# Kernel tuning notes

Hardware: AMD Instinct MI355X
Metric: run time of the kernel (lower is better)

The kernel has to match this reference:

```python
import jax, jax.numpy as jnp
import numpy as np

N_EMBED = 1024
N_HEAD = 16
D = N_EMBED // N_HEAD
B, T = 2, 2048
EPS = 1e-5


def _layer_norm(x, w, b):
    mu = jnp.mean(x, axis=-1, keepdims=True)
    var = jnp.mean(jnp.square(x - mu), axis=-1, keepdims=True)
    return (x - mu) * jax.lax.rsqrt(var + EPS) * w + b


def setup_inputs() -> dict:
    key = jax.random.key(0)
    ks = jax.random.split(key, 13)
    E = N_EMBED
    s_attn = 1.0 / np.sqrt(E)
    s_fc = 1.0 / np.sqrt(E)
    s_proj = 1.0 / np.sqrt(4 * E)
    return {
        "x": jax.random.normal(ks[0], (B, T, E), jnp.float32),
        "ln1_w": jnp.ones((E,), jnp.float32),
        "ln1_b": jnp.ones((E,), jnp.float32),
        "w_qkv": jax.random.normal(ks[1], (E, 3 * E), jnp.float32) * s_attn,
        "b_qkv": jax.random.normal(ks[2], (3 * E,), jnp.float32) * 0.02,
        "w_o": jax.random.normal(ks[3], (E, E), jnp.float32) * s_attn,
        "b_o": jax.random.normal(ks[4], (E,), jnp.float32) * 0.02,
        "ln2_w": jnp.ones((E,), jnp.float32),
        "ln2_b": jnp.ones((E,), jnp.float32),
        "w_fc": jax.random.normal(ks[5], (E, 4 * E), jnp.float32) * s_fc,
        "b_fc": jax.random.normal(ks[6], (4 * E,), jnp.float32) * 0.02,
        "w_proj": jax.random.normal(ks[7], (4 * E, E), jnp.float32) * s_proj,
        "b_proj": jax.random.normal(ks[8], (E,), jnp.float32) * 0.02,
    }


def reference(x, ln1_w, ln1_b, w_qkv, b_qkv, w_o, b_o, ln2_w, ln2_b, w_fc, b_fc, w_proj, b_proj):
    Bb, Tt, E = x.shape
    # --- attention branch ---
    h = _layer_norm(x, ln1_w, ln1_b)
    qkv = h @ w_qkv + b_qkv                         # [B,T,3E]
    q, k, v = jnp.split(qkv, 3, axis=-1)
    q = q.reshape(Bb, Tt, N_HEAD, D).transpose(0, 2, 1, 3)  # [B,H,T,D]
    k = k.reshape(Bb, Tt, N_HEAD, D).transpose(0, 2, 1, 3)
    v = v.reshape(Bb, Tt, N_HEAD, D).transpose(0, 2, 1, 3)
    scale = 1.0 / np.sqrt(D)
    a = scale * jnp.einsum("bhqd,bhkd->bhqk", q, k)  # [B,H,T,T]
    causal = jnp.tril(jnp.ones((Tt, Tt), bool))
    a = jnp.where(causal, a, -jnp.inf)
    a = jax.nn.softmax(a, axis=-1)
    y = jnp.einsum("bhqk,bhkd->bhqd", a, v)          # [B,H,T,D]
    y = y.transpose(0, 2, 1, 3).reshape(Bb, Tt, E)
    y = y @ w_o + b_o
    x = x + y
    # --- MLP branch ---
    h = _layer_norm(x, ln2_w, ln2_b)
    h = jax.nn.gelu(h @ w_fc + b_fc, approximate=False)
    h = h @ w_proj + b_proj
    return x + h
```

## Files before the change

kernel.cpp:

```cpp
#include <hip/hip_runtime.h>
#include <cstdint>
#include <cstddef>

#define E 1024
#define TT 2048
#define NB 2
#define NH 16
#define HD 64

using u16 = unsigned short;
using bf16x8 = __attribute__((ext_vector_type(8))) __bf16;
using floatx4 = __attribute__((ext_vector_type(4))) float;
using s16x4 = __attribute__((ext_vector_type(4))) short;

__device__ __forceinline__ float b2f(u16 u) {
  unsigned int x = ((unsigned int)u) << 16;
  float f;
  __builtin_memcpy(&f, &x, 4);
  return f;
}
__device__ __forceinline__ u16 f2b(float f) {
  unsigned int x;
  __builtin_memcpy(&x, &f, 4);
  x += 0x7fffu + ((x >> 16) & 1u);
  return (u16)(x >> 16);
}
__device__ __forceinline__ u16 f2b_fast(float f) {
  unsigned int x;
  float g = f * 1.001953125f;
  __builtin_memcpy(&x, &g, 4);
  return (u16)(x >> 16);
}

__device__ __forceinline__ void async16(const u16* g, u16* l) {
  __builtin_amdgcn_global_load_lds(
      (const __attribute__((address_space(1))) unsigned int*)g,
      (__attribute__((address_space(3))) unsigned int*)l, 16, 0, 0);
}

__device__ __forceinline__ floatx4 mfma32(bf16x8 a, bf16x8 b, floatx4 c) {
  return __builtin_amdgcn_mfma_f32_16x16x32_bf16(a, b, c, 0, 0, 0);
}

__device__ __forceinline__ floatx4 mfma16(s16x4 a, s16x4 b, floatx4 c) {
#if defined(__HIP_DEVICE_COMPILE__)
  return __builtin_amdgcn_mfma_f32_16x16x16bf16_1k(a, b, c, 0, 0, 0);
#else
  return c;
#endif
}

__global__ __launch_bounds__(256) void wconv_all(
    const float* __restrict__ w0, const float* __restrict__ w1,
    const float* __restrict__ w2, const float* __restrict__ w3,
    u16* __restrict__ o0, u16* __restrict__ o1, u16* __restrict__ o2,
    u16* __restrict__ o3) {
  __shared__ float tile[32][33];
  const int t = blockIdx.x;
  const float* w;
  u16* o;
  int K, N, nx, ti;
  if (t < 3072) { w = w0; o = o0; K = 1024; N = 3072; nx = 96; ti = t; }
  else if (t < 4096) { w = w1; o = o1; K = 1024; N = 1024; nx = 32; ti = t - 3072; }
  else if (t < 8192) { w = w2; o = o2; K = 1024; N = 4096; nx = 128; ti = t - 4096; }
  else { w = w3; o = o3; K = 4096; N = 1024; nx = 32; ti = t - 8192; }
  const int n0 = (ti % nx) * 32, k0 = (ti / nx) * 32;
  const int tx = threadIdx.x, ty = threadIdx.y;
#pragma unroll
  for (int i = 0; i < 32; i += 8)
    tile[ty + i][tx] = w[(size_t)(k0 + ty + i) * N + (n0 + tx)];
  __syncthreads();
#pragma unroll
  for (int i = 0; i < 32; i += 8)
    o[(size_t)(n0 + ty + i) * K + (k0 + tx)] = f2b(tile[tx][ty + i]);
}

__global__ __launch_bounds__(256) void ln_kernel(const float* __restrict__ x,
                                                 const float* __restrict__ w,
                                                 const float* __restrict__ bvec,
                                                 u16* __restrict__ outb) {
  const int row = blockIdx.x;
  const int t = threadIdx.x;
  const float4 v = ((const float4*)(x + (size_t)row * E))[t];
  float s1 = v.x + v.y + v.z + v.w;
  float s2 = v.x * v.x + v.y * v.y + v.z * v.z + v.w * v.w;
#pragma unroll
  for (int off = 32; off > 0; off >>= 1) {
    s1 += __shfl_down(s1, off);
    s2 += __shfl_down(s2, off);
  }
  __shared__ float r1[4], r2[4];
  if ((t & 63) == 0) { r1[t >> 6] = s1; r2[t >> 6] = s2; }
  __syncthreads();
  s1 = r1[0] + r1[1] + r1[2] + r1[3];
  s2 = r2[0] + r2[1] + r2[2] + r2[3];
  const float mean = s1 * (1.f / E);
  const float var = s2 * (1.f / E) - mean * mean;
  const float rstd = rsqrtf(var + 1e-5f);
  const float4 wv = ((const float4*)w)[t];
  const float4 bv = ((const float4*)bvec)[t];
  const u16 o0 = f2b((v.x - mean) * rstd * wv.x + bv.x);
  const u16 o1 = f2b((v.y - mean) * rstd * wv.y + bv.y);
  const u16 o2 = f2b((v.z - mean) * rstd * wv.z + bv.z);
  const u16 o3 = f2b((v.w - mean) * rstd * wv.w + bv.w);
  uint2 pk;
  pk.x = (unsigned)o0 | ((unsigned)o1 << 16);
  pk.y = (unsigned)o2 | ((unsigned)o3 << 16);
  ((uint2*)(outb + (size_t)row * E))[t] = pk;
}

template <int MODE, int ROWS>
__global__ __launch_bounds__(512) void gemm_bt(const u16* __restrict__ A,
                                               const u16* __restrict__ BT,
                                               const float* __restrict__ bias,
                                               const float* __restrict__ res,
                                               void* __restrict__ outp,
                                               int M, int N, int K) {
  constexpr int NJ = (ROWS == 256) ? 4 : 2;
  __shared__ __align__(16) u16 As[2][ROWS * 32];
  __shared__ __align__(16) u16 Bs[2][128 * 32];
  const int tid = threadIdx.x;
  const int wave = tid >> 6, lane = tid & 63;

  const int gx = gridDim.x, gy = gridDim.y;
  const int L = blockIdx.y * gx + blockIdx.x;
  const int xc = L & 7, wi = L >> 3;
  const int cpg = gx >> 2;
  const int rpg = gy >> 1;
  const int bxs = (xc >> 1) * cpg + (wi % cpg);
  const int bys = (xc & 1) * rpg + (wi / cpg);

  const int row0 = bys * ROWS, col0 = bxs * 128;
  const int wm = (ROWS == 256) ? (wave & 3) * 64 : (wave & 1) * 64;
  const int wn = (ROWS == 256) ? (wave >> 2) * 64 : (wave >> 1) * 32;
  const int r = lane & 15, qd = lane >> 4;

  floatx4 acc[4][NJ];
#pragma unroll
  for (int i = 0; i < 4; i++)
#pragma unroll
    for (int j = 0; j < NJ; j++) acc[i][j] = (floatx4){0.f, 0.f, 0.f, 0.f};

  const int cA0 = tid, cA1 = tid + 512, cB = tid;
  const u16* ApA = A + (size_t)(row0 + (cA0 >> 2)) * K + (cA0 & 3) * 8;
  const u16* ApB = A + (size_t)(row0 + (cA1 >> 2)) * K + (cA1 & 3) * 8;
  const u16* Bp = BT + (size_t)(col0 + (cB >> 2)) * K + (cB & 3) * 8;

  auto stage = [&](int kt, u16* Asb, u16* Bsb) {
    async16(ApA + kt, Asb + cA0 * 8);
    if (ROWS == 256) async16(ApB + kt, Asb + cA1 * 8);
    async16(Bp + kt, Bsb + cB * 8);
  };
  auto compute = [&](const u16* Asb, const u16* Bsb) {
    bf16x8 af[4], bfr[NJ];
#pragma unroll
    for (int i = 0; i < 4; i++)
      af[i] = *(const bf16x8*)&Asb[(wm + i * 16 + r) * 32 + qd * 8];
#pragma unroll
    for (int j = 0; j < NJ; j++)
      bfr[j] = *(const bf16x8*)&Bsb[(wn + j * 16 + r) * 32 + qd * 8];
#pragma unroll
    for (int i = 0; i < 4; i++)
#pragma unroll
      for (int j = 0; j < NJ; j++)
        acc[i][j] = mfma32(af[i], bfr[j], acc[i][j]);
  };

  const int nIter = K >> 5;
  stage(0, As[0], Bs[0]);
  for (int t = 0; t < nIter; t++) {
    const int tb = t & 1;
    if (t + 1 < nIter) {
      stage((t + 1) * 32, As[tb ^ 1], Bs[tb ^ 1]);
      if (ROWS == 256)
        asm volatile("s_waitcnt vmcnt(3)" ::: "memory");
      else
        asm volatile("s_waitcnt vmcnt(2)" ::: "memory");
    } else {
      asm volatile("s_waitcnt vmcnt(0)" ::: "memory");
    }
    asm volatile("s_barrier" ::: "memory");
    compute(As[tb], Bs[tb]);
    asm volatile("s_barrier" ::: "memory");
  }

#pragma unroll
  for (int i = 0; i < 4; i++) {
#pragma unroll
    for (int j = 0; j < NJ; j++) {
      const int col = col0 + wn + j * 16 + r;
      const float bc = bias[col];
      if (MODE == 3) {
        u16* base = (u16*)outp;
        const int rowb = row0 + wm + i * 16 + qd * 4;
        if (col < 2048) {
          const size_t cb =
              (col < 1024) ? (size_t)col : ((size_t)4096 * 1024 + (col - 1024));
#pragma unroll
          for (int rr = 0; rr < 4; rr++)
            base[cb + (size_t)(rowb + rr) * 1024] = f2b(acc[i][j][rr] + bc);
        } else {
          ushort4 pk;
          pk.x = f2b(acc[i][j][0] + bc);
          pk.y = f2b(acc[i][j][1] + bc);
          pk.z = f2b(acc[i][j][2] + bc);
          pk.w = f2b(acc[i][j][3] + bc);
          *(ushort4*)(base + (size_t)8 * 1024 * 1024 +
                      (size_t)(col - 2048) * 4096 + rowb) = pk;
        }
      } else {
#pragma unroll
        for (int rr = 0; rr < 4; rr++) {
          const int row = row0 + wm + i * 16 + qd * 4 + rr;
          const float v = acc[i][j][rr] + bc;
          const size_t idx = (size_t)row * N + col;
          if (MODE == 0) {
            ((u16*)outp)[idx] = f2b(v);
          } else if (MODE == 1) {
            ((float*)outp)[idx] = v + res[idx];
          } else {
            const float z = 1.5957691216f * v * (1.f + 0.044715f * v * v);
            const float g = v / (1.f + __expf(-z));
            ((u16*)outp)[idx] = f2b(g);
          }
        }
      }
    }
  }
}

__global__ __launch_bounds__(512) void gemm_ks(const u16* __restrict__ A,
                                               const u16* __restrict__ BT,
                                               const float* __restrict__ bias,
                                               const float* __restrict__ res,
                                               float* __restrict__ outp,
                                               int M, int N, int K) {
  __shared__ __align__(16) u16 As[4][2][128 * 32];
  __shared__ __align__(16) u16 Bs[4][2][128 * 32];
  const int tid = threadIdx.x;
  const int wave = tid >> 6, lane = tid & 63;

  const int gx = gridDim.x, gy = gridDim.y;
  const int L = blockIdx.y * gx + blockIdx.x;
  const int xc = L & 7, wi = L >> 3;
  const int cpg = gx >> 2, rpg = gy >> 1;
  const int bxs = (xc >> 1) * cpg + (wi % cpg);
  const int bys = (xc & 1) * rpg + (wi / cpg);

  const int row0 = bys * 128, col0 = bxs * 128;
  const int kg = wave >> 2;
  const int wm = (wave & 1) * 64, wn = ((wave >> 1) & 1) * 64;
  const int r = lane & 15, qd = lane >> 4;

  floatx4 acc[4][4];
#pragma unroll
  for (int i = 0; i < 4; i++)
#pragma unroll
    for (int j = 0; j < 4; j++) acc[i][j] = (floatx4){0.f, 0.f, 0.f, 0.f};

  const int arow = tid >> 2, aslot = (tid & 3) * 8;
  const u16* Ap = A + (size_t)(row0 + arow) * K + aslot;
  const u16* Bp = BT + (size_t)(col0 + arow) * K + aslot;

  auto stage = [&](int s, int d) {
    const int k0 = s * 64;
    async16(Ap + k0, &As[d][0][tid * 8]);
    async16(Ap + k0 + 32, &As[d][1][tid * 8]);
    async16(Bp + k0, &Bs[d][0][tid * 8]);
    async16(Bp + k0 + 32, &Bs[d][1][tid * 8]);
  };
  auto compute = [&](int d) {
    bf16x8 af[4], bfr[4];
#pragma unroll
    for (int i = 0; i < 4; i++)
      af[i] = *(const bf16x8*)&As[d][kg][(wm + i * 16 + r) * 32 + qd * 8];
#pragma unroll
    for (int j = 0; j < 4; j++)
      bfr[j] = *(const bf16x8*)&Bs[d][kg][(wn + j * 16 + r) * 32 + qd * 8];
#pragma unroll
    for (int i = 0; i < 4; i++)
#pragma unroll
      for (int j = 0; j < 4; j++)
        acc[i][j] = mfma32(af[i], bfr[j], acc[i][j]);
  };

  const int nT = K >> 6;
  stage(0, 0);
  stage(1, 1);
  stage(2, 2);
  for (int tt = 0; tt < nT; tt += 4) {
#pragma unroll
    for (int d = 0; d < 4; d++) {
      const int t = tt + d;
      const int rem = nT - 1 - t;
      if (rem >= 2)
        asm volatile("s_waitcnt vmcnt(8)" ::: "memory");
      else if (rem == 1)
        asm volatile("s_waitcnt vmcnt(4)" ::: "memory");
      else
        asm volatile("s_waitcnt vmcnt(0)" ::: "memory");
      asm volatile("s_barrier" ::: "memory");
      if (t + 3 < nT) stage(t + 3, (d + 3) & 3);
      compute(d);
    }
  }

  __syncthreads();
  float* S = (float*)&As[0][0][0];
  const int p = wave & 3;
  floatx4* W = (floatx4*)S + p * 1024 + lane;
  if (kg == 1) {
#pragma unroll
    for (int i = 0; i < 4; i++)
#pragma unroll
      for (int j = 0; j < 4; j++) W[(i * 4 + j) * 64] = acc[i][j];
  }
  __syncthreads();
  if (kg == 0) {
#pragma unroll
    for (int i = 0; i < 4; i++) {
#pragma unroll
      for (int j = 0; j < 4; j++) {
        const floatx4 w2 = W[(i * 4 + j) * 64];
        const int col = col0 + wn + j * 16 + r;
        const float bc = bias[col];
#pragma unroll
        for (int rr = 0; rr < 4; rr++) {
          const int row = row0 + wm + i * 16 + qd * 4 + rr;
          const size_t idx = (size_t)row * N + col;
          outp[idx] = acc[i][j][rr] + w2[rr] + bc + res[idx];
        }
      }
    }
  }
}

__global__ __launch_bounds__(512, 4) void attn_mfma(const u16* __restrict__ qb,
                                                    const u16* __restrict__ kb,
                                                    const u16* __restrict__ vtb,
                                                    u16* __restrict__ y) {
  const int bx = blockIdx.x;
  const int h = blockIdx.y, b = blockIdx.z;
  const int qt = b ? (15 - bx) : bx;
  const int tid = threadIdx.x;
  const int wave = tid >> 6, lane = tid & 63;
  const int quad = lane >> 4, r = lane & 15;
  const int wq = wave & 3;
  const int kvh = wave >> 2;

  __shared__ __align__(16) u16 lds[2 * 128 * 64 + 2 * 64 * 128];
  u16* KsB = lds;
  u16* VsB = lds + 2 * 128 * 64;

  const float C = 0.125f * 1.44269504f;
  const int qbase = qt * 128 + wq * 32;

  bf16x8 qf[2][2];
#pragma unroll
  for (int f = 0; f < 2; f++) {
    const u16* qp = qb + ((size_t)b * TT + qbase + f * 16 + r) * E + h * 64;
#pragma unroll
    for (int kh = 0; kh < 2; kh++) {
      union { bf16x8 v; u16 u[8]; } tmp;
#pragma unroll
      for (int j = 0; j < 8; j++) tmp.u[j] = f2b(b2f(qp[kh * 32 + quad * 8 + j]) * C);
      qf[f][kh] = tmp.v;
    }
  }

  floatx4 o[2][4];
#pragma unroll
  for (int f = 0; f < 2; f++)
#pragma unroll
    for (int i = 0; i < 4; i++) o[f][i] = (floatx4){0.f, 0.f, 0.f, 0.f};
  float lsum[2] = {0.f, 0.f};
  const bool mgt[4] = {(quad * 4 + 0) > r, (quad * 4 + 1) > r,
                       (quad * 4 + 2) > r, (quad * 4 + 3) > r};

  auto stageKV = [&](int it, int bi) {
    const int k0 = it * 128;
    u16* Kd = KsB + bi * (128 * 64);
    u16* Vd = VsB + bi * (64 * 128);
#pragma unroll
    for (int i = 0; i < 2; i++) {
      const int c = tid + i * 512;
      const int key = c >> 3, dc = (c & 7) ^ (key & 7);
      async16(kb + ((size_t)b * TT + k0 + key) * E + h * 64 + dc * 8, Kd + c * 8);
    }
#pragma unroll
    for (int i = 0; i < 2; i++) {
      const int c = tid + i * 512;
      const int d = c >> 4, kc = (c & 15) ^ (d & 15);
      async16(vtb + (size_t)(h * 64 + d) * (NB * TT) + b * TT + k0 + kc * 8,
              Vd + c * 8);
    }
  };

  const int nIter = qt + 1;
  stageKV(0, 0);
  for (int it = 0; it < nIter; it++) {
    if (it + 1 < nIter) {
      stageKV(it + 1, (it + 1) & 1);
      asm volatile("s_waitcnt vmcnt(4)" ::: "memory");
    } else {
      asm volatile("s_waitcnt vmcnt(0)" ::: "memory");
    }
    asm volatile("s_barrier" ::: "memory");
    const u16* Kb = KsB + (it & 1) * (128 * 64);
    const u16* Vb = VsB + (it & 1) * (64 * 128);
    const int k0 = it * 128;
    const int relA = (qbase - k0) >> 4;
    const int kTop = (relA + 1 < 7) ? (relA + 1) : 7;

#pragma unroll
    for (int kk = 0; kk < 4; kk++) {
      const int ks = kvh * 4 + kk;
      if (ks <= kTop) {
        const int key = ks * 16 + r, kx = key & 7;
        const bf16x8 kf0 = *(const bf16x8*)&Kb[key * 64 + (quad ^ kx) * 8];
        const bf16x8 kf1 = *(const bf16x8*)&Kb[key * 64 + ((4 + quad) ^ kx) * 8];
        floatx4 s0 = (floatx4){0.f, 0.f, 0.f, 0.f};
        s0 = mfma32(kf0, qf[0][0], s0);
        s0 = mfma32(kf1, qf[0][1], s0);
        floatx4 s1 = (floatx4){0.f, 0.f, 0.f, 0.f};
        s1 = mfma32(kf0, qf[1][0], s1);
        s1 = mfma32(kf1, qf[1][1], s1);

        s16x4 vf[4];
#pragma unroll
        for (int dsub = 0; dsub < 4; dsub++) {
          const int d = dsub * 16 + r;
          vf[dsub] = *(const s16x4*)&Vb[d * 128 + ((2 * ks + (quad >> 1)) ^ r) * 8 +
                                        (quad & 1) * 4];
        }

#pragma unroll
        for (int f = 0; f < 2; f++) {
          const floatx4 sv = (f == 0) ? s0 : s1;
          const int rel = relA + f;
          if (ks <= rel) {
            float p0 = exp2f(sv[0]);
            float p1 = exp2f(sv[1]);
            float p2 = exp2f(sv[2]);
            float p3 = exp2f(sv[3]);
            if (ks == rel) {
              if (mgt[0]) p0 = 0.f;
              if (mgt[1]) p1 = 0.f;
              if (mgt[2]) p2 = 0.f;
              if (mgt[3]) p3 = 0.f;
            }
            lsum[f] += p0 + p1 + p2 + p3;
            s16x4 pk;
            pk[0] = (short)f2b_fast(p0);
            pk[1] = (short)f2b_fast(p1);
            pk[2] = (short)f2b_fast(p2);
            pk[3] = (short)f2b_fast(p3);
#pragma unroll
            for (int dsub = 0; dsub < 4; dsub++)
              o[f][dsub] = mfma16(pk, vf[dsub], o[f][dsub]);
          }
        }
      }
    }
    asm volatile("s_barrier" ::: "memory");
  }

  floatx4* W = (floatx4*)(float*)lds + wq * 576 + lane;
  if (kvh == 1) {
#pragma unroll
    for (int f = 0; f < 2; f++)
#pragma unroll
      for (int dsub = 0; dsub < 4; dsub++) W[(f * 4 + dsub) * 64] = o[f][dsub];
    W[8 * 64] = (floatx4){lsum[0], lsum[1], 0.f, 0.f};
  }
  __syncthreads();
  if (kvh == 0) {
    const floatx4 ls2 = W[8 * 64];
#pragma unroll
    for (int f = 0; f < 2; f++) {
      float lv = lsum[f] + ((f == 0) ? ls2[0] : ls2[1]);
      lv += __shfl_xor(lv, 16);
      lv += __shfl_xor(lv, 32);
      float linv[4];
#pragma unroll
      for (int rr = 0; rr < 4; rr++) linv[rr] = 1.f / __shfl(lv, quad * 4 + rr);
#pragma unroll
      for (int dsub = 0; dsub < 4; dsub++) {
        const floatx4 o2 = W[(f * 4 + dsub) * 64];
#pragma unroll
        for (int rr = 0; rr < 4; rr++) {
          const size_t row = (size_t)b * TT + qbase + f * 16 + quad * 4 + rr;
          y[row * E + h * 64 + dsub * 16 + r] =
              f2b((o[f][dsub][rr] + o2[rr]) * linv[rr]);
        }
      }
    }
  }
}

extern "C" void kernel_launch(void* const* d_in, const int* in_sizes, int n_in,
                              void* d_out, int out_size, void* d_ws, size_t ws_size,
                              hipStream_t stream) {
  (void)in_sizes; (void)n_in; (void)out_size; (void)ws_size;
  const float* x      = (const float*)d_in[0];
  const float* ln1w   = (const float*)d_in[1];
  const float* ln1b   = (const float*)d_in[2];
  const float* w_qkv  = (const float*)d_in[3];
  const float* b_qkv  = (const float*)d_in[4];
  const float* w_o    = (const float*)d_in[5];
  const float* b_o    = (const float*)d_in[6];
  const float* ln2w   = (const float*)d_in[7];
  const float* ln2b   = (const float*)d_in[8];
  const float* w_fc   = (const float*)d_in[9];
  const float* b_fc   = (const float*)d_in[10];
  const float* w_proj = (const float*)d_in[11];
  const float* b_proj = (const float*)d_in[12];
  float* out = (float*)d_out;

  char* p = (char*)d_ws;
  u16* wT_qkv  = (u16*)p; p += (size_t)3072 * 1024 * 2;
  u16* wT_o    = (u16*)p; p += (size_t)1024 * 1024 * 2;
  u16* wT_fc   = (u16*)p; p += (size_t)4096 * 1024 * 2;
  u16* wT_proj = (u16*)p; p += (size_t)1024 * 4096 * 2;
  u16* hbuf    = (u16*)p; p += (size_t)4096 * 1024 * 2;
  u16* qkvb    = (u16*)p; p += (size_t)4096 * 3072 * 2;
  float* x2    = (float*)p; p += (size_t)4096 * 1024 * 4;
  u16* gbuf    = (u16*)p; p += (size_t)4096 * 4096 * 2;

  u16* qb  = qkvb;
  u16* kb  = qkvb + (size_t)4096 * 1024;
  u16* vtb = qkvb + (size_t)8 * 1024 * 1024;

  wconv_all<<<12288, dim3(32, 8), 0, stream>>>(w_qkv, w_o, w_fc, w_proj,
                                               wT_qkv, wT_o, wT_fc, wT_proj);

  ln_kernel<<<4096, 256, 0, stream>>>(x, ln1w, ln1b, hbuf);
  gemm_bt<3, 256><<<dim3(3072 / 128, 4096 / 256), 512, 0, stream>>>(
      hbuf, wT_qkv, b_qkv, nullptr, qkvb, 4096, 3072, 1024);
  attn_mfma<<<dim3(16, NH, NB), 512, 0, stream>>>(qb, kb, vtb, hbuf);
  gemm_ks<<<dim3(1024 / 128, 4096 / 128), 512, 0, stream>>>(
      hbuf, wT_o, b_o, x, x2, 4096, 1024, 1024);
  ln_kernel<<<4096, 256, 0, stream>>>(x2, ln2w, ln2b, hbuf);
  gemm_bt<2, 256><<<dim3(4096 / 128, 4096 / 256), 512, 0, stream>>>(
      hbuf, wT_fc, b_fc, nullptr, gbuf, 4096, 4096, 1024);
  gemm_ks<<<dim3(1024 / 128, 4096 / 128), 512, 0, stream>>>(
      gbuf, wT_proj, b_proj, x2, out, 4096, 1024, 4096);
}
```

Baseline: 319.1 us.

## Split-K the output-projection GEMMs across grid z with atomic accumulation

The gemm_ks kernel now splits K in half across blockIdx.z, doubling the block count for the N=1024 GEMMs (from 256 to 512 blocks). Partial results are combined with float atomicAdd into zero-initialised outputs, with bias and residual added only by the kz==0 half, which requires two extra memsets. The LDS pipeline also drops from four buffers to two, with an extra barrier per k-step, to cut shared memory use. The intent is better occupancy on the many-CU GPU, at the cost of atomic traffic, memset bandwidth, a shallower prefetch and non-deterministic summation order.

```diff
diff --git a/kernel.cpp b/kernel.cpp
--- a/kernel.cpp
+++ b/kernel.cpp
@@ -235,10 +235,11 @@
                                                const float* __restrict__ res,
                                                float* __restrict__ outp,
                                                int M, int N, int K) {
-  __shared__ __align__(16) u16 As[4][2][128 * 32];
-  __shared__ __align__(16) u16 Bs[4][2][128 * 32];
+  __shared__ __align__(16) u16 lds[4 * 128 * 64];
   const int tid = threadIdx.x;
   const int wave = tid >> 6, lane = tid & 63;
+  const int kz = blockIdx.z;
+  const int Kb = K >> 1;
 
   const int gx = gridDim.x, gy = gridDim.y;
   const int L = blockIdx.y * gx + blockIdx.x;
@@ -259,24 +260,28 @@
     for (int j = 0; j < 4; j++) acc[i][j] = (floatx4){0.f, 0.f, 0.f, 0.f};
 
   const int arow = tid >> 2, aslot = (tid & 3) * 8;
-  const u16* Ap = A + (size_t)(row0 + arow) * K + aslot;
-  const u16* Bp = BT + (size_t)(col0 + arow) * K + aslot;
+  const u16* Ap = A + (size_t)(row0 + arow) * K + kz * Kb + aslot;
+  const u16* Bp = BT + (size_t)(col0 + arow) * K + kz * Kb + aslot;
 
   auto stage = [&](int s, int d) {
     const int k0 = s * 64;
-    async16(Ap + k0, &As[d][0][tid * 8]);
-    async16(Ap + k0 + 32, &As[d][1][tid * 8]);
-    async16(Bp + k0, &Bs[d][0][tid * 8]);
-    async16(Bp + k0 + 32, &Bs[d][1][tid * 8]);
+    u16* Ad = lds + d * (128 * 64);
+    u16* Bd = lds + (2 + d) * (128 * 64);
+    async16(Ap + k0, Ad + tid * 8);
+    async16(Ap + k0 + 32, Ad + 128 * 32 + tid * 8);
+    async16(Bp + k0, Bd + tid * 8);
+    async16(Bp + k0 + 32, Bd + 128 * 32 + tid * 8);
   };
   auto compute = [&](int d) {
+    const u16* Ad = lds + d * (128 * 64) + kg * (128 * 32);
+    const u16* Bd = lds + (2 + d) * (128 * 64) + kg * (128 * 32);
     bf16x8 af[4], bfr[4];
 #pragma unroll
     for (int i = 0; i < 4; i++)
-      af[i] = *(const bf16x8*)&As[d][kg][(wm + i * 16 + r) * 32 + qd * 8];
+      af[i] = *(const bf16x8*)&Ad[(wm + i * 16 + r) * 32 + qd * 8];
 #pragma unroll
     for (int j = 0; j < 4; j++)
-      bfr[j] = *(const bf16x8*)&Bs[d][kg][(wn + j * 16 + r) * 32 + qd * 8];
+      bfr[j] = *(const bf16x8*)&Bd[(wn + j * 16 + r) * 32 + qd * 8];
 #pragma unroll
     for (int i = 0; i < 4; i++)
 #pragma unroll
@@ -284,29 +289,23 @@
         acc[i][j] = mfma32(af[i], bfr[j], acc[i][j]);
   };
 
-  const int nT = K >> 6;
+  const int nT = Kb >> 6;
   stage(0, 0);
-  stage(1, 1);
-  stage(2, 2);
-  for (int tt = 0; tt < nT; tt += 4) {
-#pragma unroll
-    for (int d = 0; d < 4; d++) {
-      const int t = tt + d;
-      const int rem = nT - 1 - t;
-      if (rem >= 2)
-        asm volatile("s_waitcnt vmcnt(8)" ::: "memory");
-      else if (rem == 1)
-        asm volatile("s_waitcnt vmcnt(4)" ::: "memory");
-      else
-        asm volatile("s_waitcnt vmcnt(0)" ::: "memory");
-      asm volatile("s_barrier" ::: "memory");
-      if (t + 3 < nT) stage(t + 3, (d + 3) & 3);
-      compute(d);
-    }
+  for (int t = 0; t < nT; t++) {
+    const int d = t & 1;
+    if (t + 1 < nT) {
+      stage(t + 1, d ^ 1);
+      asm volatile("s_waitcnt vmcnt(4)" ::: "memory");
+    } else {
+      asm volatile("s_waitcnt vmcnt(0)" ::: "memory");
+    }
+    asm volatile("s_barrier" ::: "memory");
+    compute(d);
+    asm volatile("s_barrier" ::: "memory");
   }
 
   __syncthreads();
-  float* S = (float*)&As[0][0][0];
+  float* S = (float*)lds;
   const int p = wave & 3;
   floatx4* W = (floatx4*)S + p * 1024 + lane;
   if (kg == 1) {
@@ -328,7 +327,9 @@
         for (int rr = 0; rr < 4; rr++) {
           const int row = row0 + wm + i * 16 + qd * 4 + rr;
           const size_t idx = (size_t)row * N + col;
-          outp[idx] = acc[i][j][rr] + w2[rr] + bc + res[idx];
+          float v = acc[i][j][rr] + w2[rr];
+          if (kz == 0) v += bc + res[idx];
+          atomicAdd(&outp[idx], v);
         }
       }
     }
@@ -531,6 +532,9 @@
   u16* kb  = qkvb + (size_t)4096 * 1024;
   u16* vtb = qkvb + (size_t)8 * 1024 * 1024;
 
+  hipMemsetAsync(x2, 0, (size_t)4096 * 1024 * 4, stream);
+  hipMemsetAsync(out, 0, (size_t)4096 * 1024 * 4, stream);
+
   wconv_all<<<12288, dim3(32, 8), 0, stream>>>(w_qkv, w_o, w_fc, w_proj,
                                                wT_qkv, wT_o, wT_fc, wT_proj);
 
@@ -538,11 +542,11 @@
   gemm_bt<3, 256><<<dim3(3072 / 128, 4096 / 256), 512, 0, stream>>>(
       hbuf, wT_qkv, b_qkv, nullptr, qkvb, 4096, 3072, 1024);
   attn_mfma<<<dim3(16, NH, NB), 512, 0, stream>>>(qb, kb, vtb, hbuf);
-  gemm_ks<<<dim3(1024 / 128, 4096 / 128), 512, 0, stream>>>(
+  gemm_ks<<<dim3(1024 / 128, 4096 / 128, 2), 512, 0, stream>>>(
       hbuf, wT_o, b_o, x, x2, 4096, 1024, 1024);
   ln_kernel<<<4096, 256, 0, stream>>>(x2, ln2w, ln2b, hbuf);
   gemm_bt<2, 256><<<dim3(4096 / 128, 4096 / 256), 512, 0, stream>>>(
       hbuf, wT_fc, b_fc, nullptr, gbuf, 4096, 4096, 1024);
-  gemm_ks<<<dim3(1024 / 128, 4096 / 128), 512, 0, stream>>>(
+  gemm_ks<<<dim3(1024 / 128, 4096 / 128, 2), 512, 0, stream>>>(
       gbuf, wT_proj, b_proj, x2, out, 4096, 1024, 4096);
 }
```

Measured after the change: 365.6 us. +14.6%, slower.
